# Performance work log

Hardware: AMD Instinct MI355X
Metric: run time of the kernel (lower is better)

## Reference

```python
import jax, jax.numpy as jnp
import numpy as np

SLOPE_IN = 0.01  # F.leaky_relu default in the wrapper
SLOPE = 0.2      # DGCNN convention inside EdgeConv blocks
K = 40           # num_points -> k nearest neighbors
LOW = 16         # lowest_size: decoder starting grid
DOM = 128        # domain_size: output grid


def lrelu(x, s):
    return jnp.where(x >= 0, x, s * x)


def conv2d(x, w, b, stride, pad):
    y = jax.lax.conv_general_dilated(x, w, stride, pad,
                                     dimension_numbers=('NCHW', 'OIHW', 'NCHW'))
    return y + b[None, :, None, None]


def knn_idx(x, k):
    # x: (B,C,N) -> (B,N,k) indices of k nearest neighbors (incl. self)
    xx = jnp.sum(x * x, axis=1)                   # (B,N)
    inner = jnp.einsum('bcn,bcm->bnm', x, x)      # (B,N,N)
    neg_d = 2.0 * inner - xx[:, :, None] - xx[:, None, :]
    _, idx = jax.lax.top_k(neg_d, k)
    return idx


def graph_feature(x, idx):
    # x: (B,C,N), idx: (B,N,k) -> (B,2C,N,k): concat(neighbor - center, center)
    nbr = jax.vmap(lambda xf, i: xf[:, i])(x, idx)   # (B,C,N,k)
    ctr = jnp.broadcast_to(x[..., None], nbr.shape)
    return jnp.concatenate([nbr - ctr, ctr], axis=1)


def edge_conv(x, w, b, k):
    # dynamic graph: recompute kNN on current features
    idx = knn_idx(x, k)
    f = graph_feature(x, idx)                                      # (B,2C,N,k)
    h = jnp.einsum('oc,bcnk->bonk', w, f) + b[None, :, None, None]
    return jnp.max(lrelu(h, SLOPE), axis=-1)                       # (B,O,N)


def up2(x):
    return jnp.repeat(jnp.repeat(x, 2, axis=2), 2, axis=3)


def setup_inputs() -> dict:
    key = jax.random.key(0)
    ks = jax.random.split(key, 16)

    def w(k, shape, fan_in):
        return jax.random.normal(k, shape, jnp.float32) / np.float32(np.sqrt(fan_in))

    z = lambda n: jnp.zeros((n,), jnp.float32)
    return {
        'x':  jax.random.normal(ks[0], (2, 10, 2048), jnp.float32),
        'Wc': w(ks[1], (1, 1, 5, 3), 15),      'bc': z(1),
        'W1': w(ks[2], (64, 4), 4),            'b1': z(64),
        'W2': w(ks[3], (64, 128), 128),        'b2': z(64),
        'W3': w(ks[4], (128, 128), 128),       'b3': z(128),
        'W4': w(ks[5], (256, 256), 256),       'b4': z(256),
        'W5': w(ks[6], (1024, 512), 512),      'b5': z(1024),
        'Wfc': w(ks[7], (LOW * LOW * 64, 1024), 1024), 'bfc': z(LOW * LOW * 64),
        'Wd1': w(ks[8], (32, 64, 3, 3), 64 * 9),  'bd1': z(32),
        'Wd2': w(ks[9], (16, 32, 3, 3), 32 * 9),  'bd2': z(16),
        'Wd3': w(ks[10], (1, 16, 3, 3), 16 * 9),  'bd3': z(1),
    }


def reference(x, Wc, bc, W1, b1, W2, b2, W3, b3, W4, b4, W5, b5,
              Wfc, bfc, Wd1, bd1, Wd2, bd2, Wd3, bd3):
    # prefix: conv2d (5,3)/(5,1) + leaky_relu -> (B,1,2,N) -> point coords (B,2,N)
    h = conv2d(x[:, None, :, :], Wc, bc, (5, 1), ((0, 0), (1, 1)))
    h = lrelu(h, SLOPE_IN)[:, 0]                         # (B,2,N)
    # dynamic-graph EdgeConv stack
    x1 = edge_conv(h, W1, b1, K)                         # (B,64,N)
    x2 = edge_conv(x1, W2, b2, K)                        # (B,64,N)
    x3 = edge_conv(x2, W3, b3, K)                        # (B,128,N)
    x4 = edge_conv(x3, W4, b4, K)                        # (B,256,N)
    cat = jnp.concatenate([x1, x2, x3, x4], axis=1)      # (B,512,N)
    g = lrelu(jnp.einsum('oc,bcn->bon', W5, cat) + b5[None, :, None], SLOPE)
    g = jnp.max(g, axis=-1)                              # (B,1024) global feature
    d = lrelu(g @ Wfc.T + bfc, SLOPE).reshape(-1, 64, LOW, LOW)
    d = lrelu(conv2d(up2(d), Wd1, bd1, (1, 1), ((1, 1), (1, 1))), SLOPE)
    d = lrelu(conv2d(up2(d), Wd2, bd2, (1, 1), ((1, 1), (1, 1))), SLOPE)
    d = conv2d(up2(d), Wd3, bd3, (1, 1), ((1, 1), (1, 1)))
    return d
```

## Files before the change

### kernel.cpp

```cpp
#include <hip/hip_runtime.h>
#include <hip/hip_bf16.h>

#define N_PTS 2048
#define BATCH 2
#define KNN 40

typedef __attribute__((ext_vector_type(8))) short bf16x8;
typedef __attribute__((ext_vector_type(16))) float f32x16;

__device__ __forceinline__ float lrelu(float v, float s) {
    return v >= 0.f ? v : s * v;
}

__global__ void prefix_kernel(const float* __restrict__ x, const float* __restrict__ Wc,
                              const float* __restrict__ bc, float* __restrict__ H) {
    int t = blockIdx.x * 256 + threadIdx.x;
    if (t >= BATCH * N_PTS) return;
    int b = t >> 11, n = t & 2047;
    #pragma unroll
    for (int oh = 0; oh < 2; ++oh) {
        float acc = bc[0];
        #pragma unroll
        for (int kh = 0; kh < 5; ++kh) {
            const float* xr = x + ((size_t)b * 10 + oh * 5 + kh) * N_PTS;
            #pragma unroll
            for (int kw = 0; kw < 3; ++kw) {
                int nn = n + kw - 1;
                if (nn >= 0 && nn < N_PTS) acc += xr[nn] * Wc[kh * 3 + kw];
            }
        }
        H[(size_t)t * 2 + oh] = lrelu(acc, 0.01f);
    }
}

__global__ __launch_bounds__(256) void gram_small_kernel(const float* __restrict__ X, long bsX,
                                                         long nstride,
                                                         float* __restrict__ negd) {
    __shared__ float AsT[2][68];
    __shared__ float BsT[2][68];
    __shared__ float xxr[64];
    __shared__ float xxc[64];
    int bz = blockIdx.z;
    const float* Xb = X + (size_t)bz * bsX;
    float* nd = negd + (size_t)bz * nstride;
    int tid = threadIdx.x;
    int r0 = blockIdx.y * 64, c0 = blockIdx.x * 64;
    int ty = tid >> 4, tx = tid & 15;
    if (tid < 128) {
        int r = tid >> 1, c = tid & 1;
        AsT[c][r] = Xb[(size_t)(r0 + r) * 2 + c];
        BsT[c][r] = Xb[(size_t)(c0 + r) * 2 + c];
        int v = (tid < 64) ? (r0 + tid) : (c0 + tid - 64);
        float x0 = Xb[(size_t)v * 2], x1 = Xb[(size_t)v * 2 + 1];
        float s = 0.f;
        s += x0 * x0;
        s += x1 * x1;
        if (tid < 64) xxr[tid] = s; else xxc[tid - 64] = s;
    }
    __syncthreads();
    float acc[4][4] = {};
    #pragma unroll
    for (int k = 0; k < 2; ++k) {
        float4 a = *(const float4*)&AsT[k][ty * 4];
        float4 b = *(const float4*)&BsT[k][tx * 4];
        #pragma unroll
        for (int i = 0; i < 4; ++i)
            #pragma unroll
            for (int j = 0; j < 4; ++j)
                acc[i][j] += (&a.x)[i] * (&b.x)[j];
    }
    #pragma unroll
    for (int i = 0; i < 4; ++i) {
        int r = r0 + ty * 4 + i;
        float xr = xxr[ty * 4 + i];
        #pragma unroll
        for (int j = 0; j < 4; ++j) {
            int c = c0 + tx * 4 + j;
            nd[(size_t)r * N_PTS + c] = 2.0f * acc[i][j] - xr - xxc[tx * 4 + j];
        }
    }
}

template<int C, int STAGE>
__global__ __launch_bounds__(256) void gram_mfma_kernel(
        const short* __restrict__ Xh, const short* __restrict__ Xl, long bsX, int S,
        const float* __restrict__ xx, long xxstride,
        float* __restrict__ negd, long nstride) {
    constexpr int NCH = C / 16;
    __shared__ float xr_s[128];
    __shared__ float xc_s[128];
    int bz = blockIdx.z;
    const short* Ah = Xh + (size_t)bz * bsX;
    const short* Al = Xl + (size_t)bz * bsX;
    const float* xxb = xx + (size_t)bz * xxstride;
    float* nd = negd + (size_t)bz * nstride;
    int tid = threadIdx.x;
    int wave = tid >> 6, lane = tid & 63;
    int wm = wave >> 1, wn = wave & 1;
    int r0 = blockIdx.y * 128 + wm * 64;
    int c0 = blockIdx.x * 128 + wn * 64;
    int rr = lane & 31, kg = lane >> 5;
    if (tid < 128) xr_s[tid] = xxb[blockIdx.y * 128 + tid];
    else           xc_s[tid - 128] = xxb[blockIdx.x * 128 + (tid - 128)];
    const int FS = 32 * S;
    const short* pAh = Ah + (size_t)(r0 + rr) * S + kg * 8;
    const short* pAl = Al + (size_t)(r0 + rr) * S + kg * 8;
    const short* pBh = Ah + (size_t)(c0 + rr) * S + kg * 8;
    const short* pBl = Al + (size_t)(c0 + rr) * S + kg * 8;
    f32x16 a00 = {}, a01 = {}, a10 = {}, a11 = {};
    bf16x8 ah0 = *(const bf16x8*)(pAh);
    bf16x8 ah1 = *(const bf16x8*)(pAh + FS);
    bf16x8 al0 = *(const bf16x8*)(pAl);
    bf16x8 al1 = *(const bf16x8*)(pAl + FS);
    bf16x8 bh0 = *(const bf16x8*)(pBh);
    bf16x8 bh1 = *(const bf16x8*)(pBh + FS);
    bf16x8 bl0 = *(const bf16x8*)(pBl);
    bf16x8 bl1 = *(const bf16x8*)(pBl + FS);
    #pragma unroll 2
    for (int kc = 0; kc < NCH; ++kc) {
        int kn = ((kc + 1) & (NCH - 1)) * 16;
        bf16x8 nah0 = *(const bf16x8*)(pAh + kn);
        bf16x8 nah1 = *(const bf16x8*)(pAh + kn + FS);
        bf16x8 nal0 = *(const bf16x8*)(pAl + kn);
        bf16x8 nal1 = *(const bf16x8*)(pAl + kn + FS);
        bf16x8 nbh0 = *(const bf16x8*)(pBh + kn);
        bf16x8 nbh1 = *(const bf16x8*)(pBh + kn + FS);
        bf16x8 nbl0 = *(const bf16x8*)(pBl + kn);
        bf16x8 nbl1 = *(const bf16x8*)(pBl + kn + FS);
        a00 = __builtin_amdgcn_mfma_f32_32x32x16_bf16(ah0, bh0, a00, 0, 0, 0);
        a00 = __builtin_amdgcn_mfma_f32_32x32x16_bf16(ah0, bl0, a00, 0, 0, 0);
        a00 = __builtin_amdgcn_mfma_f32_32x32x16_bf16(al0, bh0, a00, 0, 0, 0);
        a01 = __builtin_amdgcn_mfma_f32_32x32x16_bf16(ah0, bh1, a01, 0, 0, 0);
        a01 = __builtin_amdgcn_mfma_f32_32x32x16_bf16(ah0, bl1, a01, 0, 0, 0);
        a01 = __builtin_amdgcn_mfma_f32_32x32x16_bf16(al0, bh1, a01, 0, 0, 0);
        a10 = __builtin_amdgcn_mfma_f32_32x32x16_bf16(ah1, bh0, a10, 0, 0, 0);
        a10 = __builtin_amdgcn_mfma_f32_32x32x16_bf16(ah1, bl0, a10, 0, 0, 0);
        a10 = __builtin_amdgcn_mfma_f32_32x32x16_bf16(al1, bh0, a10, 0, 0, 0);
        a11 = __builtin_amdgcn_mfma_f32_32x32x16_bf16(ah1, bh1, a11, 0, 0, 0);
        a11 = __builtin_amdgcn_mfma_f32_32x32x16_bf16(ah1, bl1, a11, 0, 0, 0);
        a11 = __builtin_amdgcn_mfma_f32_32x32x16_bf16(al1, bh1, a11, 0, 0, 0);
        ah0 = nah0; ah1 = nah1; al0 = nal0; al1 = nal1;
        bh0 = nbh0; bh1 = nbh1; bl0 = nbl0; bl1 = nbl1;
    }
    __syncthreads();
    int colF = lane & 31;
    int hi4 = (lane >> 5) * 4;
    #pragma unroll
    for (int f = 0; f < 4; ++f) {
        int fm = f >> 1, fn = f & 1;
        int cIn = wn * 64 + fn * 32 + colF;
        float xc = xc_s[cIn];
        float* ndr = nd + (size_t)(blockIdx.y * 128) * N_PTS + blockIdx.x * 128 + cIn;
        #pragma unroll
        for (int reg = 0; reg < 16; ++reg) {
            float av = (f == 0) ? a00[reg] : (f == 1) ? a01[reg] : (f == 2) ? a10[reg] : a11[reg];
            int rIn = wm * 64 + fm * 32 + (reg & 3) + 8 * (reg >> 2) + hi4;
            ndr[(size_t)rIn * N_PTS] = 2.0f * av - xr_s[rIn] - xc;
        }
    }
}

template<int STAGE>
__global__ __launch_bounds__(256) void topk_kernel(const float* __restrict__ negd, long nstride,
                                                   int* __restrict__ idx_out) {
    __shared__ unsigned hist[2048];
    __shared__ unsigned cand[2048];
    __shared__ unsigned wsum[4];
    __shared__ unsigned sc[4];
    __shared__ unsigned tieb;
    int bz = blockIdx.y;
    int n = blockIdx.x;
    int tid = threadIdx.x;
    int wave = tid >> 6, lane = tid & 63;
    const float* row = negd + (size_t)bz * nstride + (size_t)n * N_PTS;
    float4 v0 = ((const float4*)row)[tid];
    float4 v1 = ((const float4*)row)[tid + 256];
    unsigned k0[4], k1[4];
    #pragma unroll
    for (int e = 0; e < 4; ++e) {
        unsigned u = __float_as_uint((&v0.x)[e]);
        k0[e] = (u & 0x80000000u) ? ~u : (u | 0x80000000u);
        u = __float_as_uint((&v1.x)[e]);
        k1[e] = (u & 0x80000000u) ? ~u : (u | 0x80000000u);
    }
    for (int i = tid; i < 2048; i += 256) hist[i] = 0u;
    if (tid == 0) { sc[2] = 0u; sc[3] = 0u; }
    __syncthreads();
    #pragma unroll
    for (int e = 0; e < 4; ++e) {
        atomicAdd(&hist[k0[e] >> 21], 1u);
        atomicAdd(&hist[k1[e] >> 21], 1u);
    }
    __syncthreads();
    unsigned r = KNN;
    {
        unsigned chunk = 0;
        #pragma unroll
        for (int q = 0; q < 8; ++q) chunk += hist[tid * 8 + q];
        unsigned s = chunk;
        #pragma unroll
        for (int off = 1; off < 64; off <<= 1) {
            unsigned v = __shfl_down(s, off);
            if (lane + off < 64) s += v;
        }
        if (lane == 0) wsum[wave] = s;
        __syncthreads();
        unsigned add = 0;
        for (int w = wave + 1; w < 4; ++w) add += wsum[w];
        unsigned St = s + add, Sn = St - chunk;
        if (St >= r && Sn < r) { sc[0] = (unsigned)tid; sc[1] = r - Sn; }
        __syncthreads();
        if (tid == 0) {
            int c = (int)sc[0]; unsigned rc = sc[1];
            unsigned cum = 0; int b = c * 8 + 7;
            for (;; --b) { cum += hist[b]; if (cum >= rc) break; }
            sc[0] = (unsigned)b; sc[1] = rc - (cum - hist[b]);
        }
        __syncthreads();
    }
    unsigned p1 = sc[0]; r = sc[1];
    __syncthreads();
    for (int i = tid; i < 2048; i += 256) hist[i] = 0u;
    __syncthreads();
    int* out = idx_out + ((size_t)bz * N_PTS + n) * KNN;
    #pragma unroll
    for (int h = 0; h < 2; ++h) {
        #pragma unroll
        for (int e = 0; e < 4; ++e) {
            unsigned u = (h == 0) ? k0[e] : k1[e];
            int j = (tid + h * 256) * 4 + e;
            unsigned b = u >> 21;
            if (b > p1) {
                out[atomicAdd(&sc[2], 1u)] = j;
            } else if (b == p1) {
                unsigned low = u & 0x1FFFFFu;
                cand[atomicAdd(&sc[3], 1u)] = (low << 11) | (unsigned)j;
                atomicAdd(&hist[low >> 10], 1u);
            }
        }
    }
    __syncthreads();
    int cnt = (int)sc[3];
    {
        unsigned chunk = 0;
        #pragma unroll
        for (int q = 0; q < 8; ++q) chunk += hist[tid * 8 + q];
        unsigned s = chunk;
        #pragma unroll
        for (int off = 1; off < 64; off <<= 1) {
            unsigned v = __shfl_down(s, off);
            if (lane + off < 64) s += v;
        }
        if (lane == 0) wsum[wave] = s;
        __syncthreads();
        unsigned add = 0;
        for (int w = wave + 1; w < 4; ++w) add += wsum[w];
        unsigned St = s + add, Sn = St - chunk;
        if (St >= r && Sn < r) { sc[0] = (unsigned)tid; sc[1] = r - Sn; }
        __syncthreads();
        if (tid == 0) {
            int c = (int)sc[0]; unsigned rc = sc[1];
            unsigned cum = 0; int b = c * 8 + 7;
            for (;; --b) { cum += hist[b]; if (cum >= rc) break; }
            sc[0] = (unsigned)b; sc[1] = rc - (cum - hist[b]);
        }
        __syncthreads();
    }
    unsigned b2 = sc[0]; r = sc[1];
    __syncthreads();
    for (int i = tid; i < 1024; i += 256) hist[i] = 0u;
    __syncthreads();
    for (int i = tid; i < cnt; i += 256) {
        unsigned p = cand[i];
        if ((p >> 21) == b2) atomicAdd(&hist[(p >> 11) & 0x3FFu], 1u);
    }
    __syncthreads();
    {
        unsigned chunk = 0;
        #pragma unroll
        for (int q = 0; q < 4; ++q) chunk += hist[tid * 4 + q];
        unsigned s = chunk;
        #pragma unroll
        for (int off = 1; off < 64; off <<= 1) {
            unsigned v = __shfl_down(s, off);
            if (lane + off < 64) s += v;
        }
        if (lane == 0) wsum[wave] = s;
        __syncthreads();
        unsigned add = 0;
        for (int w = wave + 1; w < 4; ++w) add += wsum[w];
        unsigned St = s + add, Sn = St - chunk;
        if (St >= r && Sn < r) { sc[0] = (unsigned)tid; sc[1] = r - Sn; }
        __syncthreads();
        if (tid == 0) {
            int c = (int)sc[0]; unsigned rc = sc[1];
            unsigned cum = 0; int b = c * 4 + 3;
            for (;; --b) { cum += hist[b]; if (cum >= rc) break; }
            sc[0] = (unsigned)b; sc[1] = rc - (cum - hist[b]);
        }
        __syncthreads();
    }
    unsigned Tlow = (b2 << 10) | sc[0];
    unsigned r3 = sc[1];
    __syncthreads();
    for (int i = tid; i < cnt; i += 256) {
        unsigned p = cand[i];
        if ((p >> 11) > Tlow) out[atomicAdd(&sc[2], 1u)] = (int)(p & 0x7FFu);
    }
    __syncthreads();
    int last = -1;
    for (unsigned t = 0; t < r3; ++t) {
        unsigned m = 0xFFFFFFFFu;
        for (int i = tid; i < cnt; i += 256) {
            unsigned p = cand[i];
            if ((p >> 11) == Tlow) {
                int j = (int)(p & 0x7FFu);
                if (j > last && (unsigned)j < m) m = (unsigned)j;
            }
        }
        hist[tid] = m;
        __syncthreads();
        for (int st = 128; st >= 1; st >>= 1) {
            if (tid < st) hist[tid] = min(hist[tid], hist[tid + st]);
            __syncthreads();
        }
        if (tid == 0) { out[KNN - (int)r3 + (int)t] = (int)hist[0]; tieb = hist[0]; }
        __syncthreads();
        last = (int)tieb;
    }
}

template<int C, int O, int STAGE>
__global__ __launch_bounds__(256) void ya_z_kernel(const float* __restrict__ X, int S, long bsX,
                                                   const float* __restrict__ W,
                                                   const float* __restrict__ bias,
                                                   float* __restrict__ YaT, float* __restrict__ ZT) {
    constexpr int KC = (C < 32) ? C : 32;
    __shared__ float Xs[16][KC + 1];
    __shared__ float WaS[KC][64];
    __shared__ float WbS[KC][64];
    int b = blockIdx.z;
    const float* Xb = X + (size_t)b * bsX;
    int n0 = blockIdx.x * 16, o0 = blockIdx.y * 64;
    int tid = threadIdx.x, ty = tid >> 4, tx = tid & 15;
    float aa[4] = {}, ab[4] = {};
    for (int k0 = 0; k0 < C; k0 += KC) {
        __syncthreads();
        for (int i = tid; i < 16 * KC; i += 256) {
            int rw = i / KC, c = i % KC;
            Xs[rw][c] = Xb[(size_t)(n0 + rw) * S + k0 + c];
        }
        for (int i = tid; i < 64 * KC; i += 256) {
            int rw = i / KC, c = i % KC;
            int scol = rw ^ ((c & 15) << 2);
            WaS[c][scol] = W[(size_t)(o0 + rw) * 2 * C + k0 + c];
            WbS[c][scol] = W[(size_t)(o0 + rw) * 2 * C + C + k0 + c];
        }
        __syncthreads();
        #pragma unroll
        for (int k = 0; k < KC; ++k) {
            float xv = Xs[ty][k];
            int m = (k & 15) << 2;
            float4 wa = *(const float4*)&WaS[k][(tx * 4) ^ m];
            float4 wb = *(const float4*)&WbS[k][(tx * 4) ^ m];
            #pragma unroll
            for (int j = 0; j < 4; ++j) {
                aa[j] += xv * (&wa.x)[j];
                ab[j] += xv * (&wb.x)[j];
            }
        }
    }
    int n = n0 + ty;
    float4 ya, zt;
    #pragma unroll
    for (int j = 0; j < 4; ++j) {
        int o = o0 + tx * 4 + j;
        (&ya.x)[j] = aa[j];
        (&zt.x)[j] = ab[j] - aa[j] + bias[o];
    }
    size_t off = ((size_t)b * N_PTS + n) * O + o0 + tx * 4;
    *(float4*)&YaT[off] = ya;
    *(float4*)&ZT[off] = zt;
}

template<int O, int STAGE, int AUX>
__global__ __launch_bounds__(256) void edge_reduce_kernel(const float* __restrict__ YaT,
                                                          const float* __restrict__ ZT,
                                                          const int* __restrict__ IDX,
                                                          float* __restrict__ CATp,
                                                          short* __restrict__ CATh,
                                                          short* __restrict__ CATl,
                                                          float* __restrict__ XX, int coloff) {
    constexpr int TPR = O / 4;
    int b = blockIdx.y;
    int tid = threadIdx.x;
    int n = blockIdx.x * (256 / TPR) + tid / TPR;
    int o = (tid % TPR) * 4;
    const float* Ya_b = YaT + (size_t)b * N_PTS * O;
    size_t rowoff = (size_t)b * N_PTS + n;
    float4 z = *(const float4*)&ZT[rowoff * O + o];
    const int* ir = IDX + rowoff * KNN;
    float4 acc = {-3.4e38f, -3.4e38f, -3.4e38f, -3.4e38f};
    #pragma unroll 8
    for (int k = 0; k < KNN; ++k) {
        int m = ir[k];
        float4 v = *(const float4*)&Ya_b[(size_t)m * O + o];
        acc.x = fmaxf(acc.x, lrelu(v.x + z.x, 0.2f));
        acc.y = fmaxf(acc.y, lrelu(v.y + z.y, 0.2f));
        acc.z = fmaxf(acc.z, lrelu(v.z + z.z, 0.2f));
        acc.w = fmaxf(acc.w, lrelu(v.w + z.w, 0.2f));
    }
    size_t coff = rowoff * 512 + coloff + o;
    *(float4*)&CATp[coff] = acc;
    short4 h, l;
    #pragma unroll
    for (int j = 0; j < 4; ++j) {
        float xv = (&acc.x)[j];
        __hip_bfloat16 hb = __float2bfloat16(xv);
        float hf = __bfloat162float(hb);
        __hip_bfloat16 lb = __float2bfloat16(xv - hf);
        (&h.x)[j] = *reinterpret_cast<short*>(&hb);
        (&l.x)[j] = *reinterpret_cast<short*>(&lb);
    }
    *(short4*)&CATh[coff] = h;
    *(short4*)&CATl[coff] = l;
    if (AUX) {
        float sq = acc.x * acc.x + acc.y * acc.y + acc.z * acc.z + acc.w * acc.w;
        #pragma unroll
        for (int off = 1; off < TPR; off <<= 1) sq += __shfl_xor(sq, off);
        if ((tid % TPR) == 0) XX[rowoff] = sq;
    }
}

__global__ void cvt_split_kernel(const float* __restrict__ src, short* __restrict__ hi,
                                 short* __restrict__ lo, int total4) {
    int t = blockIdx.x * 256 + threadIdx.x;
    if (t >= total4) return;
    float4 v = ((const float4*)src)[t];
    short4 h, l;
    #pragma unroll
    for (int j = 0; j < 4; ++j) {
        float xv = (&v.x)[j];
        __hip_bfloat16 hb = __float2bfloat16(xv);
        float hf = __bfloat162float(hb);
        __hip_bfloat16 lb = __float2bfloat16(xv - hf);
        (&h.x)[j] = *reinterpret_cast<short*>(&hb);
        (&l.x)[j] = *reinterpret_cast<short*>(&lb);
    }
    ((short4*)hi)[t] = h;
    ((short4*)lo)[t] = l;
}

__global__ __launch_bounds__(256) void w5max_mfma_kernel(
        const short* __restrict__ Ah, const short* __restrict__ Al,
        const short* __restrict__ Bh, const short* __restrict__ Bl,
        const float* __restrict__ b5, float* __restrict__ PART) {
    __shared__ float red[2][128];
    int b = blockIdx.z;
    int tid = threadIdx.x;
    int wave = tid >> 6, lane = tid & 63;
    int wm = wave >> 1, wn = wave & 1;
    int m0 = blockIdx.x * 128 + wm * 64;
    int o0 = blockIdx.y * 128 + wn * 64;
    int rr = lane & 31;
    int kg = lane >> 5;
    const int FS = 32 * 512;
    const short* pAh = Ah + ((size_t)b * N_PTS + m0 + rr) * 512 + kg * 8;
    const short* pAl = Al + ((size_t)b * N_PTS + m0 + rr) * 512 + kg * 8;
    const short* pBh = Bh + (size_t)(o0 + rr) * 512 + kg * 8;
    const short* pBl = Bl + (size_t)(o0 + rr) * 512 + kg * 8;
    f32x16 a00 = {}, a01 = {}, a10 = {}, a11 = {};
    bf16x8 ah0 = *(const bf16x8*)(pAh);
    bf16x8 ah1 = *(const bf16x8*)(pAh + FS);
    bf16x8 al0 = *(const bf16x8*)(pAl);
    bf16x8 al1 = *(const bf16x8*)(pAl + FS);
    bf16x8 bh0 = *(const bf16x8*)(pBh);
    bf16x8 bh1 = *(const bf16x8*)(pBh + FS);
    bf16x8 bl0 = *(const bf16x8*)(pBl);
    bf16x8 bl1 = *(const bf16x8*)(pBl + FS);
    #pragma unroll 2
    for (int kc = 0; kc < 32; ++kc) {
        int kn = ((kc + 1) & 31) * 16;
        bf16x8 nah0 = *(const bf16x8*)(pAh + kn);
        bf16x8 nah1 = *(const bf16x8*)(pAh + kn + FS);
        bf16x8 nal0 = *(const bf16x8*)(pAl + kn);
        bf16x8 nal1 = *(const bf16x8*)(pAl + kn + FS);
        bf16x8 nbh0 = *(const bf16x8*)(pBh + kn);
        bf16x8 nbh1 = *(const bf16x8*)(pBh + kn + FS);
        bf16x8 nbl0 = *(const bf16x8*)(pBl + kn);
        bf16x8 nbl1 = *(const bf16x8*)(pBl + kn + FS);
        a00 = __builtin_amdgcn_mfma_f32_32x32x16_bf16(ah0, bh0, a00, 0, 0, 0);
        a00 = __builtin_amdgcn_mfma_f32_32x32x16_bf16(ah0, bl0, a00, 0, 0, 0);
        a00 = __builtin_amdgcn_mfma_f32_32x32x16_bf16(al0, bh0, a00, 0, 0, 0);
        a01 = __builtin_amdgcn_mfma_f32_32x32x16_bf16(ah0, bh1, a01, 0, 0, 0);
        a01 = __builtin_amdgcn_mfma_f32_32x32x16_bf16(ah0, bl1, a01, 0, 0, 0);
        a01 = __builtin_amdgcn_mfma_f32_32x32x16_bf16(al0, bh1, a01, 0, 0, 0);
        a10 = __builtin_amdgcn_mfma_f32_32x32x16_bf16(ah1, bh0, a10, 0, 0, 0);
        a10 = __builtin_amdgcn_mfma_f32_32x32x16_bf16(ah1, bl0, a10, 0, 0, 0);
        a10 = __builtin_amdgcn_mfma_f32_32x32x16_bf16(al1, bh0, a10, 0, 0, 0);
        a11 = __builtin_amdgcn_mfma_f32_32x32x16_bf16(ah1, bh1, a11, 0, 0, 0);
        a11 = __builtin_amdgcn_mfma_f32_32x32x16_bf16(ah1, bl1, a11, 0, 0, 0);
        a11 = __builtin_amdgcn_mfma_f32_32x32x16_bf16(al1, bh1, a11, 0, 0, 0);
        ah0 = nah0; ah1 = nah1; al0 = nal0; al1 = nal1;
        bh0 = nbh0; bh1 = nbh1; bl0 = nbl0; bl1 = nbl1;
    }
    #pragma unroll
    for (int fn = 0; fn < 2; ++fn) {
        float bo = b5[o0 + fn * 32 + rr];
        float m = -3.4e38f;
        #pragma unroll
        for (int r = 0; r < 16; ++r) {
            float v0 = (fn == 0) ? a00[r] : a01[r];
            float v1 = (fn == 0) ? a10[r] : a11[r];
            m = fmaxf(m, lrelu(v0 + bo, 0.2f));
            m = fmaxf(m, lrelu(v1 + bo, 0.2f));
        }
        m = fmaxf(m, __shfl_xor(m, 32));
        red[wm][wn * 64 + fn * 32 + rr] = m;
    }
    __syncthreads();
    if (tid < 128)
        PART[((size_t)b * 16 + blockIdx.x) * 1024 + blockIdx.y * 128 + tid] =
            fmaxf(red[0][tid], red[1][tid]);
}

__global__ void greduce_kernel(const float* __restrict__ PART, float* __restrict__ G) {
    int t = blockIdx.x * 256 + threadIdx.x;
    if (t >= BATCH * 1024) return;
    int b = t >> 10, o = t & 1023;
    const float* p = PART + (size_t)b * 16 * 1024 + o;
    float m = -3.4e38f;
    for (int nb = 0; nb < 16; ++nb) m = fmaxf(m, p[(size_t)nb * 1024]);
    G[t] = m;
}

__global__ __launch_bounds__(256) void fc_kernel(const float* __restrict__ G,
                                                 const float* __restrict__ Wfc,
                                                 const float* __restrict__ bfc,
                                                 float* __restrict__ D0) {
    __shared__ float gl[2][1024];
    int tid = threadIdx.x;
    for (int i = tid; i < 2048; i += 256) gl[i >> 10][i & 1023] = G[i];
    __syncthreads();
    int wave = tid >> 6, lane = tid & 63;
    int j = blockIdx.x * 4 + wave;
    const float* wr = Wfc + (size_t)j * 1024;
    float a0 = 0.f, a1 = 0.f;
    for (int i = lane; i < 1024; i += 64) {
        float w = wr[i];
        a0 += w * gl[0][i];
        a1 += w * gl[1][i];
    }
    #pragma unroll
    for (int off = 32; off; off >>= 1) { a0 += __shfl_xor(a0, off); a1 += __shfl_xor(a1, off); }
    if (lane == 0) {
        float bb = bfc[j];
        D0[j] = lrelu(a0 + bb, 0.2f);
        D0[16384 + j] = lrelu(a1 + bb, 0.2f);
    }
}

template<int CI, int CO, int HI, int WI, int RELU>
__global__ __launch_bounds__(256) void upconv_quad_kernel(const float* __restrict__ in,
                                                          const float* __restrict__ W,
                                                          const float* __restrict__ bias,
                                                          float* __restrict__ out) {
    const int qid = blockIdx.x * 256 + threadIdx.x;
    const int p = qid / WI, q = qid % WI;
    const int co = blockIdx.y, b = blockIdx.z;
    const int HO = HI * 2, WO = WI * 2;
    int off[3][3];
    float msk[3][3];
    #pragma unroll
    for (int r = 0; r < 3; ++r) {
        int pr = p - 1 + r;
        float rm = (pr >= 0 && pr < HI) ? 1.f : 0.f;
        int prc = min(max(pr, 0), HI - 1);
        #pragma unroll
        for (int c = 0; c < 3; ++c) {
            int qc = q - 1 + c;
            float cm = (qc >= 0 && qc < WI) ? 1.f : 0.f;
            int qcc = min(max(qc, 0), WI - 1);
            off[r][c] = prc * WI + qcc;
            msk[r][c] = rm * cm;
        }
    }
    const float* inb = in + (size_t)(b * CI) * HI * WI;
    const float* wco = W + (size_t)co * CI * 9;
    float bb = bias[co];
    float a00 = bb, a01 = bb, a10 = bb, a11 = bb;
    const int me[3] = {0, 1, 1}, mo[3] = {1, 1, 2};
    #pragma unroll 4
    for (int ci = 0; ci < CI; ++ci) {
        const float* ip = inb + (size_t)ci * HI * WI;
        const float* wp = wco + ci * 9;
        float v[3][3];
        #pragma unroll
        for (int r = 0; r < 3; ++r)
            #pragma unroll
            for (int c = 0; c < 3; ++c)
                v[r][c] = msk[r][c] * ip[off[r][c]];
        #pragma unroll
        for (int dy = 0; dy < 3; ++dy) {
            #pragma unroll
            for (int dx = 0; dx < 3; ++dx) {
                float w = wp[dy * 3 + dx];
                a00 += w * v[me[dy]][me[dx]];
                a01 += w * v[me[dy]][mo[dx]];
                a10 += w * v[mo[dy]][me[dx]];
                a11 += w * v[mo[dy]][mo[dx]];
            }
        }
    }
    if (RELU) {
        a00 = lrelu(a00, 0.2f); a01 = lrelu(a01, 0.2f);
        a10 = lrelu(a10, 0.2f); a11 = lrelu(a11, 0.2f);
    }
    float* ob = out + ((size_t)(b * CO + co) * HO + 2 * p) * WO + 2 * q;
    float2 r0 = {a00, a01}, r1 = {a10, a11};
    *(float2*)ob = r0;
    *(float2*)(ob + WO) = r1;
}

extern "C" void kernel_launch(void* const* d_in, const int* in_sizes, int n_in,
                              void* d_out, int out_size, void* d_ws, size_t ws_size,
                              hipStream_t stream) {
    const float* x   = (const float*)d_in[0];
    const float* Wc  = (const float*)d_in[1];
    const float* bc  = (const float*)d_in[2];
    const float* W1  = (const float*)d_in[3];
    const float* b1  = (const float*)d_in[4];
    const float* W2  = (const float*)d_in[5];
    const float* b2  = (const float*)d_in[6];
    const float* W3  = (const float*)d_in[7];
    const float* b3  = (const float*)d_in[8];
    const float* W4  = (const float*)d_in[9];
    const float* b4  = (const float*)d_in[10];
    const float* W5  = (const float*)d_in[11];
    const float* b5  = (const float*)d_in[12];
    const float* Wfc = (const float*)d_in[13];
    const float* bfc = (const float*)d_in[14];
    const float* Wd1 = (const float*)d_in[15];
    const float* bd1 = (const float*)d_in[16];
    const float* Wd2 = (const float*)d_in[17];
    const float* bd2 = (const float*)d_in[18];
    const float* Wd3 = (const float*)d_in[19];
    const float* bd3 = (const float*)d_in[20];
    float* out = (float*)d_out;

    const long NST = (long)N_PTS * N_PTS;
    const size_t TAIL_SZ = 12214272ull;
    const size_t NEED_BATCHED = 16809984ull + 33554432ull + TAIL_SZ;
    const bool batched = ws_size >= NEED_BATCHED;
    const size_t negd_bytes = batched ? 33554432ull : 16777216ull;

    char* ws = (char*)d_ws;
    float* Hb   = (float*)(ws + 0);
    float* CAT  = (float*)(ws + 32768);
    float* YaT  = (float*)(ws + 8421376);
    float* ZT   = (float*)(ws + 12615680);
    float* NEGD = (float*)(ws + 16809984);
    char* tail  = ws + 16809984 + negd_bytes;
    float* XX   = (float*)(tail);
    int*   IDX  = (int*)  (tail + 16384);
    float* PART = (float*)(tail + 671744);
    float* G    = (float*)(tail + 802816);
    float* D0   = (float*)(tail + 811008);
    float* DEC1 = (float*)(tail + 942080);
    float* DEC2 = (float*)(tail + 1204224);
    short* W5h  = (short*)(tail + 1728512);
    short* W5l  = (short*)(tail + 2777088);
    short* CATh = (short*)(tail + 3825664);
    short* CATl = (short*)(tail + 8019968);

    prefix_kernel<<<16, 256, 0, stream>>>(x, Wc, bc, Hb);

    if (batched) {
        gram_small_kernel<<<dim3(32, 32, 2), 256, 0, stream>>>(Hb, (long)N_PTS * 2, NST, NEGD);
        topk_kernel<1><<<dim3(N_PTS, 2), 256, 0, stream>>>(NEGD, NST, IDX);
    } else {
        for (int b = 0; b < BATCH; ++b) {
            gram_small_kernel<<<dim3(32, 32, 1), 256, 0, stream>>>(Hb + (size_t)b * N_PTS * 2, 0,
                                                                   0, NEGD);
            topk_kernel<1><<<dim3(N_PTS, 1), 256, 0, stream>>>(NEGD, 0,
                                                               IDX + (size_t)b * N_PTS * KNN);
        }
    }
    ya_z_kernel<2, 64, 1><<<dim3(128, 1, BATCH), 256, 0, stream>>>(Hb, 2, (long)N_PTS * 2,
                                                                   W1, b1, YaT, ZT);
    edge_reduce_kernel<64, 1, 1><<<dim3(128, BATCH), 256, 0, stream>>>(YaT, ZT, IDX, CAT,
                                                                       CATh, CATl, XX, 0);

    if (batched) {
        gram_mfma_kernel<64, 2><<<dim3(16, 16, 2), 256, 0, stream>>>(
            CATh + 0, CATl + 0, (long)N_PTS * 512, 512, XX, N_PTS, NEGD, NST);
        topk_kernel<2><<<dim3(N_PTS, 2), 256, 0, stream>>>(NEGD, NST, IDX);
    } else {
        for (int b = 0; b < BATCH; ++b) {
            gram_mfma_kernel<64, 2><<<dim3(16, 16, 1), 256, 0, stream>>>(
                CATh + 0 + (size_t)b * N_PTS * 512, CATl + 0 + (size_t)b * N_PTS * 512, 0, 512,
                XX + b * N_PTS, 0, NEGD, 0);
            topk_kernel<2><<<dim3(N_PTS, 1), 256, 0, stream>>>(NEGD, 0,
                                                               IDX + (size_t)b * N_PTS * KNN);
        }
    }
    ya_z_kernel<64, 64, 2><<<dim3(128, 1, BATCH), 256, 0, stream>>>(CAT + 0, 512,
                                                                    (long)N_PTS * 512,
                                                                    W2, b2, YaT, ZT);
    edge_reduce_kernel<64, 2, 1><<<dim3(128, BATCH), 256, 0, stream>>>(YaT, ZT, IDX, CAT,
                                                                       CATh, CATl, XX, 64);

    if (batched) {
        gram_mfma_kernel<64, 3><<<dim3(16, 16, 2), 256, 0, stream>>>(
            CATh + 64, CATl + 64, (long)N_PTS * 512, 512, XX, N_PTS, NEGD, NST);
        topk_kernel<3><<<dim3(N_PTS, 2), 256, 0, stream>>>(NEGD, NST, IDX);
    } else {
        for (int b = 0; b < BATCH; ++b) {
            gram_mfma_kernel<64, 3><<<dim3(16, 16, 1), 256, 0, stream>>>(
                CATh + 64 + (size_t)b * N_PTS * 512, CATl + 64 + (size_t)b * N_PTS * 512, 0, 512,
                XX + b * N_PTS, 0, NEGD, 0);
            topk_kernel<3><<<dim3(N_PTS, 1), 256, 0, stream>>>(NEGD, 0,
                                                               IDX + (size_t)b * N_PTS * KNN);
        }
    }
    ya_z_kernel<64, 128, 3><<<dim3(128, 2, BATCH), 256, 0, stream>>>(CAT + 64, 512,
                                                                     (long)N_PTS * 512,
                                                                     W3, b3, YaT, ZT);
    edge_reduce_kernel<128, 3, 1><<<dim3(256, BATCH), 256, 0, stream>>>(YaT, ZT, IDX, CAT,
                                                                        CATh, CATl, XX, 128);

    if (batched) {
        gram_mfma_kernel<128, 4><<<dim3(16, 16, 2), 256, 0, stream>>>(
            CATh + 128, CATl + 128, (long)N_PTS * 512, 512, XX, N_PTS, NEGD, NST);
        topk_kernel<4><<<dim3(N_PTS, 2), 256, 0, stream>>>(NEGD, NST, IDX);
    } else {
        for (int b = 0; b < BATCH; ++b) {
            gram_mfma_kernel<128, 4><<<dim3(16, 16, 1), 256, 0, stream>>>(
                CATh + 128 + (size_t)b * N_PTS * 512, CATl + 128 + (size_t)b * N_PTS * 512, 0, 512,
                XX + b * N_PTS, 0, NEGD, 0);
            topk_kernel<4><<<dim3(N_PTS, 1), 256, 0, stream>>>(NEGD, 0,
                                                               IDX + (size_t)b * N_PTS * KNN);
        }
    }
    ya_z_kernel<128, 256, 4><<<dim3(128, 4, BATCH), 256, 0, stream>>>(CAT + 128, 512,
                                                                      (long)N_PTS * 512,
                                                                      W4, b4, YaT, ZT);
    edge_reduce_kernel<256, 4, 0><<<dim3(512, BATCH), 256, 0, stream>>>(YaT, ZT, IDX, CAT,
                                                                        CATh, CATl, XX, 256);

    cvt_split_kernel<<<(1024 * 512 / 4 + 255) / 256, 256, 0, stream>>>(
        W5, W5h, W5l, 1024 * 512 / 4);
    w5max_mfma_kernel<<<dim3(16, 8, BATCH), 256, 0, stream>>>(CATh, CATl, W5h, W5l, b5, PART);
    greduce_kernel<<<8, 256, 0, stream>>>(PART, G);
    fc_kernel<<<4096, 256, 0, stream>>>(G, Wfc, bfc, D0);

    upconv_quad_kernel<64, 32, 16, 16, 1><<<dim3(1, 32, BATCH), 256, 0, stream>>>(D0, Wd1, bd1,
                                                                                  DEC1);
    upconv_quad_kernel<32, 16, 32, 32, 1><<<dim3(4, 16, BATCH), 256, 0, stream>>>(DEC1, Wd2, bd2,
                                                                                  DEC2);
    upconv_quad_kernel<16, 1, 64, 64, 0><<<dim3(16, 1, BATCH), 256, 0, stream>>>(DEC2, Wd3, bd3,
                                                                                 out);
}
```

Before: 347.0 us.

## Co-schedule independent gram and ya_z work in shared horizontal-fused launches

Independent kernels are merged into single launches that dispatch on block index. The gram-matrix work for each EdgeConv stage now shares a grid with the Ya/Z projection for the same stage, and the prefix conv shares one with the W5 bf16 hi/lo split. This removes several kernel launches and lets the two independent workloads fill the GPU together instead of running one after another. In exchange, each fused kernel reserves the larger of the two shared-memory footprints, and the branch means both code paths are compiled into one kernel, which can raise register use and lower occupancy.

```diff
diff --git a/kernel.cpp b/kernel.cpp
--- a/kernel.cpp
+++ b/kernel.cpp
@@ -12,9 +12,15 @@
     return v >= 0.f ? v : s * v;
 }
 
-__global__ void prefix_kernel(const float* __restrict__ x, const float* __restrict__ Wc,
-                              const float* __restrict__ bc, float* __restrict__ H) {
-    int t = blockIdx.x * 256 + threadIdx.x;
+constexpr int yaz_smem_bytes(int C) {
+    return 16 * ((C < 32 ? C : 32) + 1) * 4 + 2 * (C < 32 ? C : 32) * 64 * 4;
+}
+
+__device__ __forceinline__ void prefix_body(int fb, const float* __restrict__ x,
+                                            const float* __restrict__ Wc,
+                                            const float* __restrict__ bc,
+                                            float* __restrict__ H) {
+    int t = fb * 256 + threadIdx.x;
     if (t >= BATCH * N_PTS) return;
     int b = t >> 11, n = t & 2047;
     #pragma unroll
@@ -33,18 +39,48 @@
     }
 }
 
-__global__ __launch_bounds__(256) void gram_small_kernel(const float* __restrict__ X, long bsX,
-                                                         long nstride,
-                                                         float* __restrict__ negd) {
-    __shared__ float AsT[2][68];
-    __shared__ float BsT[2][68];
-    __shared__ float xxr[64];
-    __shared__ float xxc[64];
-    int bz = blockIdx.z;
+__device__ __forceinline__ void cvt_body(int t, const float* __restrict__ src,
+                                         short* __restrict__ hi, short* __restrict__ lo,
+                                         int total4) {
+    if (t >= total4) return;
+    float4 v = ((const float4*)src)[t];
+    short4 h, l;
+    #pragma unroll
+    for (int j = 0; j < 4; ++j) {
+        float xv = (&v.x)[j];
+        __hip_bfloat16 hb = __float2bfloat16(xv);
+        float hf = __bfloat162float(hb);
+        __hip_bfloat16 lb = __float2bfloat16(xv - hf);
+        (&h.x)[j] = *reinterpret_cast<short*>(&hb);
+        (&l.x)[j] = *reinterpret_cast<short*>(&lb);
+    }
+    ((short4*)hi)[t] = h;
+    ((short4*)lo)[t] = l;
+}
+
+__global__ __launch_bounds__(256) void prefix_cvt_kernel(const float* __restrict__ x,
+                                                         const float* __restrict__ Wc,
+                                                         const float* __restrict__ bc,
+                                                         float* __restrict__ H,
+                                                         const float* __restrict__ W5,
+                                                         short* __restrict__ W5h,
+                                                         short* __restrict__ W5l) {
+    int fb = blockIdx.x;
+    if (fb < 16) prefix_body(fb, x, Wc, bc, H);
+    else cvt_body((fb - 16) * 256 + threadIdx.x, W5, W5h, W5l, 1024 * 512 / 4);
+}
+
+__device__ __forceinline__ void gram_small_body(int bx, int by, int bz, char* smem,
+                                                const float* __restrict__ X, long bsX,
+                                                long nstride, float* __restrict__ negd) {
+    float (*AsT)[68] = (float(*)[68])smem;
+    float (*BsT)[68] = (float(*)[68])(smem + 2 * 68 * 4);
+    float* xxr = (float*)(smem + 4 * 68 * 4);
+    float* xxc = xxr + 64;
     const float* Xb = X + (size_t)bz * bsX;
     float* nd = negd + (size_t)bz * nstride;
     int tid = threadIdx.x;
-    int r0 = blockIdx.y * 64, c0 = blockIdx.x * 64;
+    int r0 = by * 64, c0 = bx * 64;
     int ty = tid >> 4, tx = tid & 15;
     if (tid < 128) {
         int r = tid >> 1, c = tid & 1;
@@ -81,15 +117,14 @@
     }
 }
 
-template<int C, int STAGE>
-__global__ __launch_bounds__(256) void gram_mfma_kernel(
+template<int C>
+__device__ __forceinline__ void gram_mfma_body(int bx, int by, int bz, char* smem,
         const short* __restrict__ Xh, const short* __restrict__ Xl, long bsX, int S,
         const float* __restrict__ xx, long xxstride,
         float* __restrict__ negd, long nstride) {
     constexpr int NCH = C / 16;
-    __shared__ float xr_s[128];
-    __shared__ float xc_s[128];
-    int bz = blockIdx.z;
+    float* xr_s = (float*)smem;
+    float* xc_s = xr_s + 128;
     const short* Ah = Xh + (size_t)bz * bsX;
     const short* Al = Xl + (size_t)bz * bsX;
     const float* xxb = xx + (size_t)bz * xxstride;
@@ -97,11 +132,11 @@
     int tid = threadIdx.x;
     int wave = tid >> 6, lane = tid & 63;
     int wm = wave >> 1, wn = wave & 1;
-    int r0 = blockIdx.y * 128 + wm * 64;
-    int c0 = blockIdx.x * 128 + wn * 64;
+    int r0 = by * 128 + wm * 64;
+    int c0 = bx * 128 + wn * 64;
     int rr = lane & 31, kg = lane >> 5;
-    if (tid < 128) xr_s[tid] = xxb[blockIdx.y * 128 + tid];
-    else           xc_s[tid - 128] = xxb[blockIdx.x * 128 + (tid - 128)];
+    if (tid < 128) xr_s[tid] = xxb[by * 128 + tid];
+    else           xc_s[tid - 128] = xxb[bx * 128 + (tid - 128)];
     const int FS = 32 * S;
     const short* pAh = Ah + (size_t)(r0 + rr) * S + kg * 8;
     const short* pAl = Al + (size_t)(r0 + rr) * S + kg * 8;
@@ -150,7 +185,7 @@
         int fm = f >> 1, fn = f & 1;
         int cIn = wn * 64 + fn * 32 + colF;
         float xc = xc_s[cIn];
-        float* ndr = nd + (size_t)(blockIdx.y * 128) * N_PTS + blockIdx.x * 128 + cIn;
+        float* ndr = nd + (size_t)(by * 128) * N_PTS + bx * 128 + cIn;
         #pragma unroll
         for (int reg = 0; reg < 16; ++reg) {
             float av = (f == 0) ? a00[reg] : (f == 1) ? a01[reg] : (f == 2) ? a10[reg] : a11[reg];
@@ -158,6 +193,130 @@
             ndr[(size_t)rIn * N_PTS] = 2.0f * av - xr_s[rIn] - xc;
         }
     }
+}
+
+template<int C, int O>
+__device__ __forceinline__ void ya_z_body(int bx, int by, int bz, char* smem,
+        const float* __restrict__ X, int S, long bsX,
+        const float* __restrict__ W, const float* __restrict__ bias,
+        float* __restrict__ YaT, float* __restrict__ ZT) {
+    constexpr int KC = (C < 32) ? C : 32;
+    float (*Xs)[KC + 1] = (float(*)[KC + 1])smem;
+    float (*WaS)[64] = (float(*)[64])(smem + 16 * (KC + 1) * 4);
+    float (*WbS)[64] = (float(*)[64])(smem + 16 * (KC + 1) * 4 + KC * 64 * 4);
+    const float* Xb = X + (size_t)bz * bsX;
+    int n0 = bx * 16, o0 = by * 64;
+    int tid = threadIdx.x, ty = tid >> 4, tx = tid & 15;
+    float aa[4] = {}, ab[4] = {};
+    for (int k0 = 0; k0 < C; k0 += KC) {
+        __syncthreads();
+        for (int i = tid; i < 16 * KC; i += 256) {
+            int rw = i / KC, c = i % KC;
+            Xs[rw][c] = Xb[(size_t)(n0 + rw) * S + k0 + c];
+        }
+        for (int i = tid; i < 64 * KC; i += 256) {
+            int rw = i / KC, c = i % KC;
+            int scol = rw ^ ((c & 15) << 2);
+            WaS[c][scol] = W[(size_t)(o0 + rw) * 2 * C + k0 + c];
+            WbS[c][scol] = W[(size_t)(o0 + rw) * 2 * C + C + k0 + c];
+        }
+        __syncthreads();
+        #pragma unroll
+        for (int k = 0; k < KC; ++k) {
+            float xv = Xs[ty][k];
+            int m = (k & 15) << 2;
+            float4 wa = *(const float4*)&WaS[k][(tx * 4) ^ m];
+            float4 wb = *(const float4*)&WbS[k][(tx * 4) ^ m];
+            #pragma unroll
+            for (int j = 0; j < 4; ++j) {
+                aa[j] += xv * (&wa.x)[j];
+                ab[j] += xv * (&wb.x)[j];
+            }
+        }
+    }
+    int n = n0 + ty;
+    float4 ya, zt;
+    #pragma unroll
+    for (int j = 0; j < 4; ++j) {
+        int o = o0 + tx * 4 + j;
+        (&ya.x)[j] = aa[j];
+        (&zt.x)[j] = ab[j] - aa[j] + bias[o];
+    }
+    size_t off = ((size_t)bz * N_PTS + n) * O + o0 + tx * 4;
+    *(float4*)&YaT[off] = ya;
+    *(float4*)&ZT[off] = zt;
+}
+
+__global__ __launch_bounds__(256) void stage1_par_kernel(const float* __restrict__ Hb,
+                                                         long bsX, long nstride,
+                                                         float* __restrict__ negd,
+                                                         const float* __restrict__ W1,
+                                                         const float* __restrict__ b1,
+                                                         float* __restrict__ YaT,
+                                                         float* __restrict__ ZT) {
+    __shared__ __align__(16) char smem[1664];
+    int fb = blockIdx.x;
+    const int NG = 32 * 32 * BATCH;
+    if (fb < NG) {
+        int bx = fb & 31, by = (fb >> 5) & 31, bz = fb >> 10;
+        gram_small_body(bx, by, bz, smem, Hb, bsX, nstride, negd);
+    } else {
+        int r = fb - NG;
+        int bx = r & 127, bz = r >> 7;
+        ya_z_body<2, 64>(bx, 0, bz, smem, Hb, 2, bsX, W1, b1, YaT, ZT);
+    }
+}
+
+template<int C, int O, int STAGE>
+__global__ __launch_bounds__(256) void stage_par_kernel(
+        const short* __restrict__ Xh, const short* __restrict__ Xl, long bsXs, int S,
+        const float* __restrict__ xx, long xxstride,
+        float* __restrict__ negd, long nstride,
+        const float* __restrict__ X, long bsX,
+        const float* __restrict__ W, const float* __restrict__ bias,
+        float* __restrict__ YaT, float* __restrict__ ZT) {
+    constexpr int SMEM = yaz_smem_bytes(C) > 1024 ? yaz_smem_bytes(C) : 1024;
+    __shared__ __align__(16) char smem[SMEM];
+    int fb = blockIdx.x;
+    const int NG = 16 * 16 * BATCH;
+    if (fb < NG) {
+        int bx = fb & 15, by = (fb >> 4) & 15, bz = fb >> 8;
+        gram_mfma_body<C>(bx, by, bz, smem, Xh, Xl, bsXs, S, xx, xxstride, negd, nstride);
+    } else {
+        int r = fb - NG;
+        constexpr int NBY = O / 64;
+        int bx = r & 127;
+        int t = r >> 7;
+        int by = t % NBY, bz = t / NBY;
+        ya_z_body<C, O>(bx, by, bz, smem, X, 512, bsX, W, bias, YaT, ZT);
+    }
+}
+
+__global__ __launch_bounds__(256) void gram_small_kernel(const float* __restrict__ X, long bsX,
+                                                         long nstride,
+                                                         float* __restrict__ negd) {
+    __shared__ __align__(16) char smem[1664];
+    gram_small_body(blockIdx.x, blockIdx.y, blockIdx.z, smem, X, bsX, nstride, negd);
+}
+
+template<int C, int STAGE>
+__global__ __launch_bounds__(256) void gram_mfma_kernel(
+        const short* __restrict__ Xh, const short* __restrict__ Xl, long bsX, int S,
+        const float* __restrict__ xx, long xxstride,
+        float* __restrict__ negd, long nstride) {
+    __shared__ __align__(16) char smem[1088];
+    gram_mfma_body<C>(blockIdx.x, blockIdx.y, blockIdx.z, smem, Xh, Xl, bsX, S, xx, xxstride,
+                      negd, nstride);
+}
+
+template<int C, int O, int STAGE>
+__global__ __launch_bounds__(256) void ya_z_kernel(const float* __restrict__ X, int S, long bsX,
+                                                   const float* __restrict__ W,
+                                                   const float* __restrict__ bias,
+                                                   float* __restrict__ YaT, float* __restrict__ ZT) {
+    constexpr int SMEM = yaz_smem_bytes(C);
+    __shared__ __align__(16) char smem[SMEM];
+    ya_z_body<C, O>(blockIdx.x, blockIdx.y, blockIdx.z, smem, X, S, bsX, W, bias, YaT, ZT);
 }
 
 template<int STAGE>
@@ -328,59 +487,6 @@
         __syncthreads();
         last = (int)tieb;
     }
-}
-
-template<int C, int O, int STAGE>
-__global__ __launch_bounds__(256) void ya_z_kernel(const float* __restrict__ X, int S, long bsX,
-                                                   const float* __restrict__ W,
-                                                   const float* __restrict__ bias,
-                                                   float* __restrict__ YaT, float* __restrict__ ZT) {
-    constexpr int KC = (C < 32) ? C : 32;
-    __shared__ float Xs[16][KC + 1];
-    __shared__ float WaS[KC][64];
-    __shared__ float WbS[KC][64];
-    int b = blockIdx.z;
-    const float* Xb = X + (size_t)b * bsX;
-    int n0 = blockIdx.x * 16, o0 = blockIdx.y * 64;
-    int tid = threadIdx.x, ty = tid >> 4, tx = tid & 15;
-    float aa[4] = {}, ab[4] = {};
-    for (int k0 = 0; k0 < C; k0 += KC) {
-        __syncthreads();
-        for (int i = tid; i < 16 * KC; i += 256) {
-            int rw = i / KC, c = i % KC;
-            Xs[rw][c] = Xb[(size_t)(n0 + rw) * S + k0 + c];
-        }
-        for (int i = tid; i < 64 * KC; i += 256) {
-            int rw = i / KC, c = i % KC;
-            int scol = rw ^ ((c & 15) << 2);
-            WaS[c][scol] = W[(size_t)(o0 + rw) * 2 * C + k0 + c];
-            WbS[c][scol] = W[(size_t)(o0 + rw) * 2 * C + C + k0 + c];
-        }
-        __syncthreads();
-        #pragma unroll
-        for (int k = 0; k < KC; ++k) {
-            float xv = Xs[ty][k];
-            int m = (k & 15) << 2;
-            float4 wa = *(const float4*)&WaS[k][(tx * 4) ^ m];
-            float4 wb = *(const float4*)&WbS[k][(tx * 4) ^ m];
-            #pragma unroll
-            for (int j = 0; j < 4; ++j) {
-                aa[j] += xv * (&wa.x)[j];
-                ab[j] += xv * (&wb.x)[j];
-            }
-        }
-    }
-    int n = n0 + ty;
-    float4 ya, zt;
-    #pragma unroll
-    for (int j = 0; j < 4; ++j) {
-        int o = o0 + tx * 4 + j;
-        (&ya.x)[j] = aa[j];
-        (&zt.x)[j] = ab[j] - aa[j] + bias[o];
-    }
-    size_t off = ((size_t)b * N_PTS + n) * O + o0 + tx * 4;
-    *(float4*)&YaT[off] = ya;
-    *(float4*)&ZT[off] = zt;
 }
 
 template<int O, int STAGE, int AUX>
@@ -430,25 +536,6 @@
         for (int off = 1; off < TPR; off <<= 1) sq += __shfl_xor(sq, off);
         if ((tid % TPR) == 0) XX[rowoff] = sq;
     }
-}
-
-__global__ void cvt_split_kernel(const float* __restrict__ src, short* __restrict__ hi,
-                                 short* __restrict__ lo, int total4) {
-    int t = blockIdx.x * 256 + threadIdx.x;
-    if (t >= total4) return;
-    float4 v = ((const float4*)src)[t];
-    short4 h, l;
-    #pragma unroll
-    for (int j = 0; j < 4; ++j) {
-        float xv = (&v.x)[j];
-        __hip_bfloat16 hb = __float2bfloat16(xv);
-        float hf = __bfloat162float(hb);
-        __hip_bfloat16 lb = __float2bfloat16(xv - hf);
-        (&h.x)[j] = *reinterpret_cast<short*>(&hb);
-        (&l.x)[j] = *reinterpret_cast<short*>(&lb);
-    }
-    ((short4*)hi)[t] = h;
-    ((short4*)lo)[t] = l;
 }
 
 __global__ __launch_bounds__(256) void w5max_mfma_kernel(
@@ -673,11 +760,32 @@
     short* CATh = (short*)(tail + 3825664);
     short* CATl = (short*)(tail + 8019968);
 
-    prefix_kernel<<<16, 256, 0, stream>>>(x, Wc, bc, Hb);
+    prefix_cvt_kernel<<<528, 256, 0, stream>>>(x, Wc, bc, Hb, W5, W5h, W5l);
 
     if (batched) {
-        gram_small_kernel<<<dim3(32, 32, 2), 256, 0, stream>>>(Hb, (long)N_PTS * 2, NST, NEGD);
+        stage1_par_kernel<<<2048 + 256, 256, 0, stream>>>(Hb, (long)N_PTS * 2, NST, NEGD,
+                                                          W1, b1, YaT, ZT);
         topk_kernel<1><<<dim3(N_PTS, 2), 256, 0, stream>>>(NEGD, NST, IDX);
+        edge_reduce_kernel<64, 1, 1><<<dim3(128, BATCH), 256, 0, stream>>>(YaT, ZT, IDX, CAT,
+                                                                           CATh, CATl, XX, 0);
+        stage_par_kernel<64, 64, 2><<<512 + 256, 256, 0, stream>>>(
+            CATh + 0, CATl + 0, (long)N_PTS * 512, 512, XX, N_PTS, NEGD, NST,
+            CAT + 0, (long)N_PTS * 512, W2, b2, YaT, ZT);
+        topk_kernel<2><<<dim3(N_PTS, 2), 256, 0, stream>>>(NEGD, NST, IDX);
+        edge_reduce_kernel<64, 2, 1><<<dim3(128, BATCH), 256, 0, stream>>>(YaT, ZT, IDX, CAT,
+                                                                           CATh, CATl, XX, 64);
+        stage_par_kernel<64, 128, 3><<<512 + 512, 256, 0, stream>>>(
+            CATh + 64, CATl + 64, (long)N_PTS * 512, 512, XX, N_PTS, NEGD, NST,
+            CAT + 64, (long)N_PTS * 512, W3, b3, YaT, ZT);
+        topk_kernel<3><<<dim3(N_PTS, 2), 256, 0, stream>>>(NEGD, NST, IDX);
+        edge_reduce_kernel<128, 3, 1><<<dim3(256, BATCH), 256, 0, stream>>>(YaT, ZT, IDX, CAT,
+                                                                            CATh, CATl, XX, 128);
+        stage_par_kernel<128, 256, 4><<<512 + 1024, 256, 0, stream>>>(
+            CATh + 128, CATl + 128, (long)N_PTS * 512, 512, XX, N_PTS, NEGD, NST,
+            CAT + 128, (long)N_PTS * 512, W4, b4, YaT, ZT);
+        topk_kernel<4><<<dim3(N_PTS, 2), 256, 0, stream>>>(NEGD, NST, IDX);
+        edge_reduce_kernel<256, 4, 0><<<dim3(512, BATCH), 256, 0, stream>>>(YaT, ZT, IDX, CAT,
+                                                                            CATh, CATl, XX, 256);
     } else {
         for (int b = 0; b < BATCH; ++b) {
             gram_small_kernel<<<dim3(32, 32, 1), 256, 0, stream>>>(Hb + (size_t)b * N_PTS * 2, 0,
@@ -685,17 +793,10 @@
             topk_kernel<1><<<dim3(N_PTS, 1), 256, 0, stream>>>(NEGD, 0,
                                                                IDX + (size_t)b * N_PTS * KNN);
         }
-    }
-    ya_z_kernel<2, 64, 1><<<dim3(128, 1, BATCH), 256, 0, stream>>>(Hb, 2, (long)N_PTS * 2,
-                                                                   W1, b1, YaT, ZT);
-    edge_reduce_kernel<64, 1, 1><<<dim3(128, BATCH), 256, 0, stream>>>(YaT, ZT, IDX, CAT,
-                                                                       CATh, CATl, XX, 0);
-
-    if (batched) {
-        gram_mfma_kernel<64, 2><<<dim3(16, 16, 2), 256, 0, stream>>>(
-            CATh + 0, CATl + 0, (long)N_PTS * 512, 512, XX, N_PTS, NEGD, NST);
-        topk_kernel<2><<<dim3(N_PTS, 2), 256, 0, stream>>>(NEGD, NST, IDX);
-    } else {
+        ya_z_kernel<2, 64, 1><<<dim3(128, 1, BATCH), 256, 0, stream>>>(Hb, 2, (long)N_PTS * 2,
+                                                                       W1, b1, YaT, ZT);
+        edge_reduce_kernel<64, 1, 1><<<dim3(128, BATCH), 256, 0, stream>>>(YaT, ZT, IDX, CAT,
+                                                                           CATh, CATl, XX, 0);
         for (int b = 0; b < BATCH; ++b) {
             gram_mfma_kernel<64, 2><<<dim3(16, 16, 1), 256, 0, stream>>>(
                 CATh + 0 + (size_t)b * N_PTS * 512, CATl + 0 + (size_t)b * N_PTS * 512, 0, 512,
@@ -703,18 +804,11 @@
             topk_kernel<2><<<dim3(N_PTS, 1), 256, 0, stream>>>(NEGD, 0,
                                                                IDX + (size_t)b * N_PTS * KNN);
         }
-    }
-    ya_z_kernel<64, 64, 2><<<dim3(128, 1, BATCH), 256, 0, stream>>>(CAT + 0, 512,
-                                                                    (long)N_PTS * 512,
-                                                                    W2, b2, YaT, ZT);
-    edge_reduce_kernel<64, 2, 1><<<dim3(128, BATCH), 256, 0, stream>>>(YaT, ZT, IDX, CAT,
-                                                                       CATh, CATl, XX, 64);
-
-    if (batched) {
-        gram_mfma_kernel<64, 3><<<dim3(16, 16, 2), 256, 0, stream>>>(
-            CATh + 64, CATl + 64, (long)N_PTS * 512, 512, XX, N_PTS, NEGD, NST);
-        topk_kernel<3><<<dim3(N_PTS, 2), 256, 0, stream>>>(NEGD, NST, IDX);
-    } else {
+        ya_z_kernel<64, 64, 2><<<dim3(128, 1, BATCH), 256, 0, stream>>>(CAT + 0, 512,
+                                                                        (long)N_PTS * 512,
+                                                                        W2, b2, YaT, ZT);
+        edge_reduce_kernel<64, 2, 1><<<dim3(128, BATCH), 256, 0, stream>>>(YaT, ZT, IDX, CAT,
+                                                                           CATh, CATl, XX, 64);
         for (int b = 0; b < BATCH; ++b) {
             gram_mfma_kernel<64, 3><<<dim3(16, 16, 1), 256, 0, stream>>>(
                 CATh + 64 + (size_t)b * N_PTS * 512, CATl + 64 + (size_t)b * N_PTS * 512, 0, 512,
@@ -722,18 +816,11 @@
             topk_kernel<3><<<dim3(N_PTS, 1), 256, 0, stream>>>(NEGD, 0,
                                                                IDX + (size_t)b * N_PTS * KNN);
         }
-    }
-    ya_z_kernel<64, 128, 3><<<dim3(128, 2, BATCH), 256, 0, stream>>>(CAT + 64, 512,
-                                                                     (long)N_PTS * 512,
-                                                                     W3, b3, YaT, ZT);
-    edge_reduce_kernel<128, 3, 1><<<dim3(256, BATCH), 256, 0, stream>>>(YaT, ZT, IDX, CAT,
-                                                                        CATh, CATl, XX, 128);
-
-    if (batched) {
-        gram_mfma_kernel<128, 4><<<dim3(16, 16, 2), 256, 0, stream>>>(
-            CATh + 128, CATl + 128, (long)N_PTS * 512, 512, XX, N_PTS, NEGD, NST);
-        topk_kernel<4><<<dim3(N_PTS, 2), 256, 0, stream>>>(NEGD, NST, IDX);
-    } else {
+        ya_z_kernel<64, 128, 3><<<dim3(128, 2, BATCH), 256, 0, stream>>>(CAT + 64, 512,
+                                                                         (long)N_PTS * 512,
+                                                                         W3, b3, YaT, ZT);
+        edge_reduce_kernel<128, 3, 1><<<dim3(256, BATCH), 256, 0, stream>>>(YaT, ZT, IDX, CAT,
+                                                                            CATh, CATl, XX, 128);
         for (int b = 0; b < BATCH; ++b) {
             gram_mfma_kernel<128, 4><<<dim3(16, 16, 1), 256, 0, stream>>>(
                 CATh + 128 + (size_t)b * N_PTS * 512, CATl + 128 + (size_t)b * N_PTS * 512, 0, 512,
@@ -741,15 +828,13 @@
             topk_kernel<4><<<dim3(N_PTS, 1), 256, 0, stream>>>(NEGD, 0,
                                                                IDX + (size_t)b * N_PTS * KNN);
         }
-    }
-    ya_z_kernel<128, 256, 4><<<dim3(128, 4, BATCH), 256, 0, stream>>>(CAT + 128, 512,
-                                                                      (long)N_PTS * 512,
-                                                                      W4, b4, YaT, ZT);
-    edge_reduce_kernel<256, 4, 0><<<dim3(512, BATCH), 256, 0, stream>>>(YaT, ZT, IDX, CAT,
-                                                                        CATh, CATl, XX, 256);
-
-    cvt_split_kernel<<<(1024 * 512 / 4 + 255) / 256, 256, 0, stream>>>(
-        W5, W5h, W5l, 1024 * 512 / 4);
+        ya_z_kernel<128, 256, 4><<<dim3(128, 4, BATCH), 256, 0, stream>>>(CAT + 128, 512,
+                                                                          (long)N_PTS * 512,
+                                                                          W4, b4, YaT, ZT);
+        edge_reduce_kernel<256, 4, 0><<<dim3(512, BATCH), 256, 0, stream>>>(YaT, ZT, IDX, CAT,
+                                                                            CATh, CATl, XX, 256);
+    }
+
     w5max_mfma_kernel<<<dim3(16, 8, BATCH), 256, 0, stream>>>(CATh, CATl, W5h, W5l, b5, PART);
     greduce_kernel<<<8, 256, 0, stream>>>(PART, G);
     fc_kernel<<<4096, 256, 0, stream>>>(G, Wfc, bfc, D0);
```

After: 347.1 us. About the same (+0.0%).
